# Optimization experiments

Measured on AMD Instinct MI355X. Metric: run time of the kernel, lower is better.

## Reference

```python
import jax, jax.numpy as jnp
import numpy as np

B, S, E, H = 2, 2048, 1024, 16
D = E // H  # head dim = 64


def setup_inputs() -> dict:
    key = jax.random.key(0)
    ks = jax.random.split(key, 9)
    sc = 0.02
    return {
        "inputs": jax.random.normal(ks[0], (B, S, E), jnp.float32),
        "Wq": jax.random.normal(ks[1], (E, E), jnp.float32) * sc,
        "bq": jnp.zeros((E,), jnp.float32),
        "Wk": jax.random.normal(ks[2], (E, E), jnp.float32) * sc,
        "bk": jnp.zeros((E,), jnp.float32),
        "Wv": jax.random.normal(ks[3], (E, E), jnp.float32) * sc,
        "bv": jnp.zeros((E,), jnp.float32),
        "Wo": jax.random.normal(ks[4], (E, E), jnp.float32) * sc,
        "bo": jnp.zeros((E,), jnp.float32),
    }


def _split_heads(x):
    # [B, S, E] -> [B, H, S, D]
    b, s, _ = x.shape
    return x.reshape(b, s, H, D).transpose(0, 2, 1, 3)


def reference(inputs, Wq, bq, Wk, bk, Wv, bv, Wo, bo):
    q = _split_heads(inputs @ Wq + bq)
    k = _split_heads(inputs @ Wk + bk)
    v = _split_heads(inputs @ Wv + bv)

    # scaled dot-product scores: [B, H, S, S]
    score = jnp.einsum("bhqd,bhkd->bhqk", q, k) / jnp.sqrt(jnp.float32(D))

    # causal mask, exactly as the original: score*mask - 10000*(1-mask)
    i = jnp.arange(S)[:, None]
    j = jnp.arange(S)[None, :]
    mask = (i >= j).astype(score.dtype)  # square case of i >= j - S + S
    score = score * mask - 10000.0 * (1.0 - mask)

    weights = jax.nn.softmax(score, axis=-1)
    attn = jnp.einsum("bhqk,bhkd->bhqd", weights, v)  # [B, H, S, D]
    attn = attn.transpose(0, 2, 1, 3).reshape(inputs.shape[0], S, E)
    return attn @ Wo + bo
```

## Files before the change

### kernel.cpp

```cpp
#include <hip/hip_runtime.h>
#include <stdint.h>

#define Bc 2
#define Sc 2048
#define Ec 1024
#define Hc 16
#define Dc 64
#define Mc (Bc*Sc)

typedef __attribute__((ext_vector_type(4))) float f32x4;
typedef __attribute__((ext_vector_type(8))) short bf16x8v;

#define SCL 0.1803368801f

__device__ __forceinline__ unsigned short f2bf(float f){
  unsigned int u = __float_as_uint(f);
  u += 0x7FFFu + ((u >> 16) & 1u);
  return (unsigned short)(u >> 16);
}

__global__ __launch_bounds__(256) void k_prep(const float* __restrict__ X,
                                              unsigned short* __restrict__ Xb,
                                              const float* __restrict__ W0, const float* __restrict__ W1,
                                              const float* __restrict__ W2, const float* __restrict__ W3,
                                              unsigned short* __restrict__ WT4){
  __shared__ float st[64][65];
  int bx = blockIdx.x, t = threadIdx.x;
  if (bx < 4096){
    int i = bx*256 + t;
    float4 v = ((const float4*)X)[i];
    ushort4 o;
    o.x = f2bf(v.x); o.y = f2bf(v.y); o.z = f2bf(v.z); o.w = f2bf(v.w);
    ((ushort4*)Xb)[i] = o;
  } else {
    int id = bx - 4096;
    int z = id >> 8, rem = id & 255;
    int k0 = (rem >> 4)*64, n0 = (rem & 15)*64;
    const float* W = (z==0)?W0 : (z==1)?W1 : (z==2)?W2 : W3;
    unsigned short* o = WT4 + (size_t)z * Ec * Ec;
    #pragma unroll
    for (int i=0;i<16;i++){ int lin=i*256+t; int r=lin>>6, c=lin&63;
      st[r][c] = W[(size_t)(k0+r)*Ec + n0+c]; }
    __syncthreads();
    #pragma unroll
    for (int i=0;i<16;i++){ int lin=i*256+t; int nn=lin>>6, kk=lin&63;
      o[(size_t)(n0+nn)*Ec + k0+kk] = f2bf(st[kk][nn]); }
  }
}

template<int MODE, int BN>
__global__ __launch_bounds__(256,4) void k_gemm(const unsigned short* __restrict__ A,
                                              const unsigned short* __restrict__ WTbase,
                                              const float* __restrict__ b0,
                                              const float* __restrict__ b1,
                                              const float* __restrict__ b2,
                                              void* __restrict__ outv){
  constexpr int NSN = BN/32;
  __shared__ unsigned short sA[2][128*32];
  __shared__ unsigned short sB[2][BN*32];
  int z = blockIdx.z;
  const unsigned short* WT = WTbase + (size_t)z * Ec * Ec;
  const float* bias = (z==0)?b0 : (z==1)?b1 : b2;
  int bm = blockIdx.y, bn = blockIdx.x;
  int t = threadIdx.x, w = t>>6, lane = t&63, quad = lane>>4, m16 = lane&15;
  int wm = w>>1, wn = w&1;
  f32x4 acc[4][NSN];
  #pragma unroll
  for (int i=0;i<4;i++)
    #pragma unroll
    for (int j=0;j<NSN;j++) acc[i][j] = (f32x4){0.f,0.f,0.f,0.f};

  auto stage = [&](int kt, int buf){
    #pragma unroll
    for (int i=0;i<2;i++){
      int cb = (w*2 + i)*64;
      int L = cb + lane;
      int row = L>>2, c = (L&3)*8;
      const unsigned short* ga = A + (size_t)(bm*128 + row)*Ec + kt*32 + c;
      __builtin_amdgcn_global_load_lds((const __attribute__((address_space(1))) void*)ga,
          (__attribute__((address_space(3))) void*)(&sA[buf][0] + cb*8), 16, 0, 0);
    }
    #pragma unroll
    for (int i=0;i<BN/64;i++){
      int cb = (w*(BN/64) + i)*64;
      int L = cb + lane;
      int row = L>>2, c = (L&3)*8;
      const unsigned short* gb = WT + (size_t)(bn*BN + row)*Ec + kt*32 + c;
      __builtin_amdgcn_global_load_lds((const __attribute__((address_space(1))) void*)gb,
          (__attribute__((address_space(3))) void*)(&sB[buf][0] + cb*8), 16, 0, 0);
    }
  };

  stage(0, 0);
  for (int kt=0; kt<Ec/32; ++kt){
    int cur = kt & 1;
    __syncthreads();
    if (kt+1 < Ec/32) stage(kt+1, cur^1);
    bf16x8v af[4], bfr[NSN];
    #pragma unroll
    for (int s=0;s<4;s++)
      af[s]  = *(const bf16x8v*)(&sA[cur][0] + (wm*64 + s*16 + m16)*32 + quad*8);
    #pragma unroll
    for (int s=0;s<NSN;s++)
      bfr[s] = *(const bf16x8v*)(&sB[cur][0] + (wn*(BN/2) + s*16 + m16)*32 + quad*8);
    #pragma unroll
    for (int sm=0;sm<4;sm++)
      #pragma unroll
      for (int sn=0;sn<NSN;sn++)
        acc[sm][sn] = __builtin_amdgcn_mfma_f32_16x16x32_bf16(af[sm], bfr[sn], acc[sm][sn], 0,0,0);
  }
  #pragma unroll
  for (int sm=0;sm<4;sm++){
    int row0 = bm*128 + wm*64 + sm*16 + quad*4;
    #pragma unroll
    for (int sn=0;sn<NSN;sn++){
      int col = bn*BN + wn*(BN/2) + sn*16 + m16;
      float bb = bias[col];
      if (MODE==0){
        unsigned short* Out = (unsigned short*)outv + (size_t)z * (size_t)Mc * Ec;
        int bidx = row0 >> 11;
        int h = col >> 6, d = col & 63;
        if (z == 2){
          int s0 = row0 & (Sc-1);
          ushort4 pk;
          pk.x = f2bf(acc[sm][sn][0] + bb);
          pk.y = f2bf(acc[sm][sn][1] + bb);
          pk.z = f2bf(acc[sm][sn][2] + bb);
          pk.w = f2bf(acc[sm][sn][3] + bb);
          *(ushort4*)(Out + (((size_t)bidx*Hc + h)*Dc + d)*Sc + s0) = pk;
        } else {
          float sc_ = (z==0) ? SCL : 1.0f;
          #pragma unroll
          for (int r=0;r<4;r++){
            int s = (row0 + r) & (Sc-1);
            Out[(((size_t)bidx*Hc + h)*Sc + s)*Dc + d] = f2bf((acc[sm][sn][r] + bb)*sc_);
          }
        }
      } else {
        float* Out = (float*)outv;
        #pragma unroll
        for (int r=0;r<4;r++)
          Out[(size_t)(row0+r)*Ec + col] = acc[sm][sn][r] + bb;
      }
    }
  }
}

__device__ __forceinline__ void attn_tile(const unsigned short* sK, const unsigned short* sVT,
                                          unsigned short* pw, bf16x8v qf0, bf16x8v qf1,
                                          bf16x8v ones, f32x4& li, f32x4* Oa,
                                          int kbase, int qw, int quad, int m16){
  int sw = m16 & 7;
  f32x4 sc[4];
  #pragma unroll
  for (int sm=0;sm<4;sm++){
    int row = sm*16 + m16;
    bf16x8v kf0 = *(const bf16x8v*)(sK + row*64 + ((quad  )^sw)*8);
    bf16x8v kf1 = *(const bf16x8v*)(sK + row*64 + ((quad+4)^sw)*8);
    f32x4 a = (f32x4){0.f,0.f,0.f,0.f};
    a = __builtin_amdgcn_mfma_f32_16x16x32_bf16(kf0, qf0, a, 0,0,0);
    a = __builtin_amdgcn_mfma_f32_16x16x32_bf16(kf1, qf1, a, 0,0,0);
    sc[sm] = a;
  }
  if (kbase + 63 > qw){
    #pragma unroll
    for (int sm=0;sm<4;sm++)
      #pragma unroll
      for (int r=0;r<4;r++){
        int kg = kbase + sm*16 + quad*4 + r;
        float p = exp2f(sc[sm][r]);
        sc[sm][r] = (kg <= qw + m16) ? p : 0.0f;
      }
  } else {
    #pragma unroll
    for (int sm=0;sm<4;sm++)
      #pragma unroll
      for (int r=0;r<4;r++) sc[sm][r] = exp2f(sc[sm][r]);
  }

  #pragma unroll
  for (int sm=0;sm<4;sm++){
    ushort4 pk;
    pk.x = f2bf(sc[sm][0]); pk.y = f2bf(sc[sm][1]);
    pk.z = f2bf(sc[sm][2]); pk.w = f2bf(sc[sm][3]);
    int chunk = sm*2 + (quad>>1);
    *(ushort4*)(pw + m16*64 + (chunk^sw)*8 + (quad&1)*4) = pk;
  }
  bf16x8v pf0 = *(const bf16x8v*)(pw + m16*64 + ((quad  )^sw)*8);
  bf16x8v pf1 = *(const bf16x8v*)(pw + m16*64 + ((quad+4)^sw)*8);

  li = __builtin_amdgcn_mfma_f32_16x16x32_bf16(pf0, ones, li, 0,0,0);
  li = __builtin_amdgcn_mfma_f32_16x16x32_bf16(pf1, ones, li, 0,0,0);

  #pragma unroll
  for (int tt=0;tt<4;tt++){
    int rowv = tt*16 + m16;
    bf16x8v vf0 = *(const bf16x8v*)(sVT + rowv*64 + ((quad  )^sw)*8);
    bf16x8v vf1 = *(const bf16x8v*)(sVT + rowv*64 + ((quad+4)^sw)*8);
    Oa[tt] = __builtin_amdgcn_mfma_f32_16x16x32_bf16(pf0, vf0, Oa[tt], 0,0,0);
    Oa[tt] = __builtin_amdgcn_mfma_f32_16x16x32_bf16(pf1, vf1, Oa[tt], 0,0,0);
  }
}

__global__ __launch_bounds__(256,2) void k_attn(const unsigned short* __restrict__ Qb,
                                                const unsigned short* __restrict__ Kb,
                                                const unsigned short* __restrict__ VTb,
                                                unsigned short* __restrict__ Ob){
  __shared__ unsigned short sK [64*64];
  __shared__ unsigned short sVT[64*64];
  __shared__ unsigned short sP [4][16*64];
  int bh = blockIdx.y;
  int qtA = (int)blockIdx.x;
  int qtB = 31 - qtA;
  size_t base = (size_t)bh * Sc * Dc;
  const unsigned short* Q  = Qb  + base;
  const unsigned short* K  = Kb  + base;
  const unsigned short* VT = VTb + base;
  int t = threadIdx.x, w = t>>6, lane = t&63, quad = lane>>4, m16 = lane&15;
  int qwA = qtA*64 + w*16;
  int qwB = qtB*64 + w*16;

  bf16x8v qA0 = *(const bf16x8v*)(Q + (size_t)(qwA + m16)*Dc + quad*8);
  bf16x8v qA1 = *(const bf16x8v*)(Q + (size_t)(qwA + m16)*Dc + 32 + quad*8);
  bf16x8v qB0 = *(const bf16x8v*)(Q + (size_t)(qwB + m16)*Dc + quad*8);
  bf16x8v qB1 = *(const bf16x8v*)(Q + (size_t)(qwB + m16)*Dc + 32 + quad*8);

  bf16x8v ones;
  #pragma unroll
  for (int i=0;i<8;i++) ones[i] = (short)0x3F80;

  f32x4 OaA[4], OaB[4];
  #pragma unroll
  for (int i=0;i<4;i++){ OaA[i] = (f32x4){0.f,0.f,0.f,0.f}; OaB[i] = (f32x4){0.f,0.f,0.f,0.f}; }
  f32x4 liA = (f32x4){0.f,0.f,0.f,0.f}, liB = (f32x4){0.f,0.f,0.f,0.f};

  unsigned short* pw = &sP[w][0];

  for (int kt=0; kt<=qtB; ++kt){
    int kbase = kt*64;
    #pragma unroll
    for (int i=0;i<2;i++){
      int cb = (w*2 + i)*64;
      int L = cb + lane;
      int row = L>>3, p = L&7, c = p ^ (row&7);
      const unsigned short* gk = K  + (size_t)(kbase+row)*Dc + c*8;
      const unsigned short* gv = VT + (size_t)row*Sc + kbase + c*8;
      __builtin_amdgcn_global_load_lds((const __attribute__((address_space(1))) void*)gk,
          (__attribute__((address_space(3))) void*)(sK + cb*8), 16, 0, 0);
      __builtin_amdgcn_global_load_lds((const __attribute__((address_space(1))) void*)gv,
          (__attribute__((address_space(3))) void*)(sVT + cb*8), 16, 0, 0);
    }
    __syncthreads();

    if (kt <= qtA)
      attn_tile(sK, sVT, pw, qA0, qA1, ones, liA, OaA, kbase, qwA, quad, m16);
    attn_tile(sK, sVT, pw, qB0, qB1, ones, liB, OaB, kbase, qwB, quad, m16);

    __syncthreads();
  }

  int b = bh >> 4, h = bh & 15;
  float iA[4], iB[4];
  #pragma unroll
  for (int r=0;r<4;r++){ iA[r] = 1.0f/liA[r]; iB[r] = 1.0f/liB[r]; }
  #pragma unroll
  for (int tt=0;tt<4;tt++)
    #pragma unroll
    for (int r=0;r<4;r++){
      int e = h*64 + tt*16 + m16;
      int sA_ = qwA + quad*4 + r;
      int sB_ = qwB + quad*4 + r;
      Ob[((size_t)b*Sc + sA_)*Ec + e] = f2bf(OaA[tt][r]*iA[r]);
      Ob[((size_t)b*Sc + sB_)*Ec + e] = f2bf(OaB[tt][r]*iB[r]);
    }
}

extern "C" void kernel_launch(void* const* d_in, const int* in_sizes, int n_in,
                              void* d_out, int out_size, void* d_ws, size_t ws_size,
                              hipStream_t stream){
  const float* X  = (const float*)d_in[0];
  const float* Wq = (const float*)d_in[1];
  const float* bq = (const float*)d_in[2];
  const float* Wk = (const float*)d_in[3];
  const float* bk = (const float*)d_in[4];
  const float* Wv = (const float*)d_in[5];
  const float* bv = (const float*)d_in[6];
  const float* Wo = (const float*)d_in[7];
  const float* bo = (const float*)d_in[8];

  uint8_t* ws = (uint8_t*)d_ws;
  unsigned short* Xb  = (unsigned short*)(ws);
  unsigned short* WT4 = (unsigned short*)(ws + (size_t)(8u<<20));
  unsigned short* QKV = (unsigned short*)(ws + (size_t)(16u<<20));
  unsigned short* ATT = (unsigned short*)(ws + (size_t)(40u<<20));

  k_prep<<<dim3(5120), 256, 0, stream>>>(X, Xb, Wq, Wk, Wv, Wo, WT4);
  k_gemm<0,64><<<dim3(16,32,3), 256, 0, stream>>>(Xb, WT4, bq, bk, bv, (void*)QKV);
  k_attn<<<dim3(16,32), 256, 0, stream>>>(QKV, QKV + (size_t)Mc*Ec, QKV + 2*(size_t)Mc*Ec, ATT);
  k_gemm<1,64><<<dim3(16,32,1), 256, 0, stream>>>(ATT, WT4 + (size_t)3*Ec*Ec, bo, bo, bo, d_out);
}
```

Before: 205.0 us.

## Fuse Q/K/V projections into one GEMM kernel sharing the input tile

Replaces the z-indexed QKV GEMM launch (three separate block sets) with a single kernel where each block computes Q, K and V for the same 128x64 output tile. The staged A tile is loaded once and reused across three weight tiles, cutting input reads from global memory and LDS by a factor of three. The block count drops from 1536 to 512. Accumulator registers triple and launch bounds fall to 2 waves per SIMD, lowering occupancy. The output GEMM becomes a dedicated non-templated kernel with the same behaviour as before.

Result: no change. 208.2 us (+1.6%).

```diff
diff --git a/kernel.cpp b/kernel.cpp
--- a/kernel.cpp
+++ b/kernel.cpp
@@ -48,27 +48,24 @@
   }
 }
 
-template<int MODE, int BN>
-__global__ __launch_bounds__(256,4) void k_gemm(const unsigned short* __restrict__ A,
-                                              const unsigned short* __restrict__ WTbase,
-                                              const float* __restrict__ b0,
-                                              const float* __restrict__ b1,
-                                              const float* __restrict__ b2,
-                                              void* __restrict__ outv){
-  constexpr int NSN = BN/32;
+__global__ __launch_bounds__(256,2) void k_qkv(const unsigned short* __restrict__ A,
+                                               const unsigned short* __restrict__ WT4,
+                                               const float* __restrict__ bq,
+                                               const float* __restrict__ bk,
+                                               const float* __restrict__ bv,
+                                               unsigned short* __restrict__ QKV){
   __shared__ unsigned short sA[2][128*32];
-  __shared__ unsigned short sB[2][BN*32];
-  int z = blockIdx.z;
-  const unsigned short* WT = WTbase + (size_t)z * Ec * Ec;
-  const float* bias = (z==0)?b0 : (z==1)?b1 : b2;
+  __shared__ unsigned short sB[2][3][64*32];
   int bm = blockIdx.y, bn = blockIdx.x;
   int t = threadIdx.x, w = t>>6, lane = t&63, quad = lane>>4, m16 = lane&15;
   int wm = w>>1, wn = w&1;
-  f32x4 acc[4][NSN];
-  #pragma unroll
-  for (int i=0;i<4;i++)
-    #pragma unroll
-    for (int j=0;j<NSN;j++) acc[i][j] = (f32x4){0.f,0.f,0.f,0.f};
+  f32x4 acc[3][4][2];
+  #pragma unroll
+  for (int z=0;z<3;z++)
+    #pragma unroll
+    for (int i=0;i<4;i++)
+      #pragma unroll
+      for (int j=0;j<2;j++) acc[z][i][j] = (f32x4){0.f,0.f,0.f,0.f};
 
   auto stage = [&](int kt, int buf){
     #pragma unroll
@@ -81,13 +78,13 @@
           (__attribute__((address_space(3))) void*)(&sA[buf][0] + cb*8), 16, 0, 0);
     }
     #pragma unroll
-    for (int i=0;i<BN/64;i++){
-      int cb = (w*(BN/64) + i)*64;
+    for (int z=0;z<3;z++){
+      int cb = w*64;
       int L = cb + lane;
       int row = L>>2, c = (L&3)*8;
-      const unsigned short* gb = WT + (size_t)(bn*BN + row)*Ec + kt*32 + c;
+      const unsigned short* gb = WT4 + (size_t)z*Ec*Ec + (size_t)(bn*64 + row)*Ec + kt*32 + c;
       __builtin_amdgcn_global_load_lds((const __attribute__((address_space(1))) void*)gb,
-          (__attribute__((address_space(3))) void*)(&sB[buf][0] + cb*8), 16, 0, 0);
+          (__attribute__((address_space(3))) void*)(&sB[buf][z][0] + cb*8), 16, 0, 0);
     }
   };
 
@@ -96,52 +93,120 @@
     int cur = kt & 1;
     __syncthreads();
     if (kt+1 < Ec/32) stage(kt+1, cur^1);
-    bf16x8v af[4], bfr[NSN];
+    bf16x8v af[4];
     #pragma unroll
     for (int s=0;s<4;s++)
-      af[s]  = *(const bf16x8v*)(&sA[cur][0] + (wm*64 + s*16 + m16)*32 + quad*8);
-    #pragma unroll
-    for (int s=0;s<NSN;s++)
-      bfr[s] = *(const bf16x8v*)(&sB[cur][0] + (wn*(BN/2) + s*16 + m16)*32 + quad*8);
-    #pragma unroll
-    for (int sm=0;sm<4;sm++)
-      #pragma unroll
-      for (int sn=0;sn<NSN;sn++)
-        acc[sm][sn] = __builtin_amdgcn_mfma_f32_16x16x32_bf16(af[sm], bfr[sn], acc[sm][sn], 0,0,0);
-  }
-  #pragma unroll
-  for (int sm=0;sm<4;sm++){
-    int row0 = bm*128 + wm*64 + sm*16 + quad*4;
-    #pragma unroll
-    for (int sn=0;sn<NSN;sn++){
-      int col = bn*BN + wn*(BN/2) + sn*16 + m16;
-      float bb = bias[col];
-      if (MODE==0){
-        unsigned short* Out = (unsigned short*)outv + (size_t)z * (size_t)Mc * Ec;
-        int bidx = row0 >> 11;
+      af[s] = *(const bf16x8v*)(&sA[cur][0] + (wm*64 + s*16 + m16)*32 + quad*8);
+    #pragma unroll
+    for (int z=0;z<3;z++){
+      bf16x8v bfr[2];
+      #pragma unroll
+      for (int s=0;s<2;s++)
+        bfr[s] = *(const bf16x8v*)(&sB[cur][z][0] + (wn*32 + s*16 + m16)*32 + quad*8);
+      #pragma unroll
+      for (int sm=0;sm<4;sm++)
+        #pragma unroll
+        for (int sn=0;sn<2;sn++)
+          acc[z][sm][sn] = __builtin_amdgcn_mfma_f32_16x16x32_bf16(af[sm], bfr[sn], acc[z][sm][sn], 0,0,0);
+    }
+  }
+  #pragma unroll
+  for (int z=0;z<3;z++){
+    const float* bias = (z==0)?bq : (z==1)?bk : bv;
+    unsigned short* Out = QKV + (size_t)z * (size_t)Mc * Ec;
+    #pragma unroll
+    for (int sm=0;sm<4;sm++){
+      int row0 = bm*128 + wm*64 + sm*16 + quad*4;
+      int bidx = row0 >> 11;
+      #pragma unroll
+      for (int sn=0;sn<2;sn++){
+        int col = bn*64 + wn*32 + sn*16 + m16;
+        float bb = bias[col];
         int h = col >> 6, d = col & 63;
         if (z == 2){
           int s0 = row0 & (Sc-1);
           ushort4 pk;
-          pk.x = f2bf(acc[sm][sn][0] + bb);
-          pk.y = f2bf(acc[sm][sn][1] + bb);
-          pk.z = f2bf(acc[sm][sn][2] + bb);
-          pk.w = f2bf(acc[sm][sn][3] + bb);
+          pk.x = f2bf(acc[z][sm][sn][0] + bb);
+          pk.y = f2bf(acc[z][sm][sn][1] + bb);
+          pk.z = f2bf(acc[z][sm][sn][2] + bb);
+          pk.w = f2bf(acc[z][sm][sn][3] + bb);
           *(ushort4*)(Out + (((size_t)bidx*Hc + h)*Dc + d)*Sc + s0) = pk;
         } else {
           float sc_ = (z==0) ? SCL : 1.0f;
           #pragma unroll
           for (int r=0;r<4;r++){
             int s = (row0 + r) & (Sc-1);
-            Out[(((size_t)bidx*Hc + h)*Sc + s)*Dc + d] = f2bf((acc[sm][sn][r] + bb)*sc_);
+            Out[(((size_t)bidx*Hc + h)*Sc + s)*Dc + d] = f2bf((acc[z][sm][sn][r] + bb)*sc_);
           }
         }
-      } else {
-        float* Out = (float*)outv;
-        #pragma unroll
-        for (int r=0;r<4;r++)
-          Out[(size_t)(row0+r)*Ec + col] = acc[sm][sn][r] + bb;
       }
+    }
+  }
+}
+
+__global__ __launch_bounds__(256,4) void k_gemm1(const unsigned short* __restrict__ A,
+                                                 const unsigned short* __restrict__ WT,
+                                                 const float* __restrict__ bias,
+                                                 float* __restrict__ Out){
+  __shared__ unsigned short sA[2][128*32];
+  __shared__ unsigned short sB[2][64*32];
+  int bm = blockIdx.y, bn = blockIdx.x;
+  int t = threadIdx.x, w = t>>6, lane = t&63, quad = lane>>4, m16 = lane&15;
+  int wm = w>>1, wn = w&1;
+  f32x4 acc[4][2];
+  #pragma unroll
+  for (int i=0;i<4;i++)
+    #pragma unroll
+    for (int j=0;j<2;j++) acc[i][j] = (f32x4){0.f,0.f,0.f,0.f};
+
+  auto stage = [&](int kt, int buf){
+    #pragma unroll
+    for (int i=0;i<2;i++){
+      int cb = (w*2 + i)*64;
+      int L = cb + lane;
+      int row = L>>2, c = (L&3)*8;
+      const unsigned short* ga = A + (size_t)(bm*128 + row)*Ec + kt*32 + c;
+      __builtin_amdgcn_global_load_lds((const __attribute__((address_space(1))) void*)ga,
+          (__attribute__((address_space(3))) void*)(&sA[buf][0] + cb*8), 16, 0, 0);
+    }
+    {
+      int cb = w*64;
+      int L = cb + lane;
+      int row = L>>2, c = (L&3)*8;
+      const unsigned short* gb = WT + (size_t)(bn*64 + row)*Ec + kt*32 + c;
+      __builtin_amdgcn_global_load_lds((const __attribute__((address_space(1))) void*)gb,
+          (__attribute__((address_space(3))) void*)(&sB[buf][0] + cb*8), 16, 0, 0);
+    }
+  };
+
+  stage(0, 0);
+  for (int kt=0; kt<Ec/32; ++kt){
+    int cur = kt & 1;
+    __syncthreads();
+    if (kt+1 < Ec/32) stage(kt+1, cur^1);
+    bf16x8v af[4], bfr[2];
+    #pragma unroll
+    for (int s=0;s<4;s++)
+      af[s]  = *(const bf16x8v*)(&sA[cur][0] + (wm*64 + s*16 + m16)*32 + quad*8);
+    #pragma unroll
+    for (int s=0;s<2;s++)
+      bfr[s] = *(const bf16x8v*)(&sB[cur][0] + (wn*32 + s*16 + m16)*32 + quad*8);
+    #pragma unroll
+    for (int sm=0;sm<4;sm++)
+      #pragma unroll
+      for (int sn=0;sn<2;sn++)
+        acc[sm][sn] = __builtin_amdgcn_mfma_f32_16x16x32_bf16(af[sm], bfr[sn], acc[sm][sn], 0,0,0);
+  }
+  #pragma unroll
+  for (int sm=0;sm<4;sm++){
+    int row0 = bm*128 + wm*64 + sm*16 + quad*4;
+    #pragma unroll
+    for (int sn=0;sn<2;sn++){
+      int col = bn*64 + wn*32 + sn*16 + m16;
+      float bb = bias[col];
+      #pragma unroll
+      for (int r=0;r<4;r++)
+        Out[(size_t)(row0+r)*Ec + col] = acc[sm][sn][r] + bb;
     }
   }
 }
@@ -295,7 +360,7 @@
   unsigned short* ATT = (unsigned short*)(ws + (size_t)(40u<<20));
 
   k_prep<<<dim3(5120), 256, 0, stream>>>(X, Xb, Wq, Wk, Wv, Wo, WT4);
-  k_gemm<0,64><<<dim3(16,32,3), 256, 0, stream>>>(Xb, WT4, bq, bk, bv, (void*)QKV);
+  k_qkv<<<dim3(16,32), 256, 0, stream>>>(Xb, WT4, bq, bk, bv, QKV);
   k_attn<<<dim3(16,32), 256, 0, stream>>>(QKV, QKV + (size_t)Mc*Ec, QKV + 2*(size_t)Mc*Ec, ATT);
-  k_gemm<1,64><<<dim3(16,32,1), 256, 0, stream>>>(ATT, WT4 + (size_t)3*Ec*Ec, bo, bo, bo, d_out);
-}
+  k_gemm1<<<dim3(16,32), 256, 0, stream>>>(ATT, WT4 + (size_t)3*Ec*Ec, bo, (float*)d_out);
+}
```
